# Performance work log

Hardware: AMD Instinct MI355X
Metric: run time of the kernel (lower is better)

The kernel has to match this reference:

```python
import jax, jax.numpy as jnp
from jax import lax
import numpy as np

# torch.sign(torch.sign(x) + 0.5): maps x<0 -> -1, x>=0 -> +1 (zeros go to +1)
def binarize(x):
    return jnp.where(x >= 0, 1.0, -1.0).astype(x.dtype)


def setup_inputs() -> dict:
    key = jax.random.key(0)
    kx, kw, kb = jax.random.split(key, 3)
    x = jax.random.normal(kx, (32, 256, 56, 56), dtype=jnp.float32)
    weight = jax.random.normal(kw, (256, 256, 3, 3), dtype=jnp.float32)
    bias = jax.random.normal(kb, (256,), dtype=jnp.float32)
    return {"x": x, "weight": weight, "bias": bias}


def reference(x, weight, bias):
    b_weight = binarize(weight)  # [O, I, kH, kW] in {-1, +1}
    b_bias = binarize(bias)      # [O] in {-1, +1}
    out = lax.conv_general_dilated(
        x, b_weight,
        window_strides=(1, 1),
        padding=((1, 1), (1, 1)),
        rhs_dilation=(1, 1),
        feature_group_count=1,
        dimension_numbers=("NCHW", "OIHW", "NCHW"),
    )
    return out + b_bias[None, :, None, None]
```

## Files before the change

kernel.cpp:

```cpp
#include <hip/hip_runtime.h>
#include <stdint.h>


#define N_IMG 32
#define C_IN  256
#define H_IN  56
#define W_IN  56
#define O_OUT 256
#define HW    (H_IN * W_IN)
#define K_RAW (C_IN * 9)

typedef int8_t i8x16 __attribute__((ext_vector_type(16)));
typedef int    i32x4 __attribute__((ext_vector_type(4)));
typedef float  f32x4 __attribute__((ext_vector_type(4)));
typedef __bf16 bf16x8 __attribute__((ext_vector_type(8)));

#define XQ_WSTR (58 * 64)
#define XQ_CSTR (58 * 58 * 64)
#define XQ_BYTES ((size_t)N_IMG * 4 * XQ_CSTR)
#define WQ_BYTES ((size_t)36 * 256 * 64)
#define AM_OFF   (XQ_BYTES + WQ_BYTES)
#define WS_NEED  (AM_OFF + 64)

#define BPITCH  80
#define BS_ROWB (58 * BPITCH)
#define APITCH  80

__global__ void amax_zero(unsigned* am) {
    if (threadIdx.x == 0 && blockIdx.x == 0) *am = 0u;
}

__global__ void amax_kernel(const float* __restrict__ x, unsigned* __restrict__ am) {
    const size_t NV = (size_t)N_IMG * C_IN * HW / 4;
    float m = 0.f;
    for (size_t i = (size_t)blockIdx.x * 256 + threadIdx.x; i < NV;
         i += (size_t)gridDim.x * 256) {
        f32x4 v = ((const f32x4*)x)[i];
        m = fmaxf(m, fmaxf(fmaxf(fabsf(v[0]), fabsf(v[1])),
                           fmaxf(fabsf(v[2]), fabsf(v[3]))));
    }
#pragma unroll
    for (int off = 32; off; off >>= 1)
        m = fmaxf(m, __shfl_down(m, off));
    __shared__ float red[4];
    if ((threadIdx.x & 63) == 0) red[threadIdx.x >> 6] = m;
    __syncthreads();
    if (threadIdx.x == 0) {
        m = fmaxf(fmaxf(red[0], red[1]), fmaxf(red[2], red[3]));
        atomicMax(am, __float_as_uint(m));
    }
}

__global__ void xtrans_q(const float* __restrict__ x, int8_t* __restrict__ xq,
                         const unsigned* __restrict__ amax_bits) {
    const int hh = blockIdx.x;
    const int cc = blockIdx.y;
    const int n  = blockIdx.z;
    const int t  = threadIdx.x;
    const int ww = t >> 2;
    const int cy = t & 3;
    if (ww >= 58) return;

    const float am    = __uint_as_float(*amax_bits);
    const float scale = 127.f / fmaxf(am, 1e-20f);

    i8x16 v;
    if (hh >= 1 && hh <= 56 && ww >= 1 && ww <= 56) {
        const float* src = x + ((size_t)n * C_IN + cc * 64 + cy * 16) * HW
                             + (hh - 1) * W_IN + (ww - 1);
#pragma unroll
        for (int j = 0; j < 16; ++j) {
            float f = src[(size_t)j * HW] * scale;
            f = fminf(fmaxf(f, -127.f), 127.f);
            v[j] = (int8_t)(int)rintf(f);
        }
    } else {
#pragma unroll
        for (int j = 0; j < 16; ++j) v[j] = 0;
    }
    *(i8x16*)(xq + ((size_t)(n * 4 + cc) * 3364 + hh * 58 + ww) * 64 + cy * 16) = v;
}

__global__ void wshuf_q(const float* __restrict__ w, int8_t* __restrict__ wq) {
    int idx = blockIdx.x * 256 + threadIdx.x;
    int cg  = idx & 3;
    int o   = (idx >> 2) & 255;
    int st  = idx >> 10;
    int tap = st % 9;
    int cc  = st / 9;
    i8x16 v;
#pragma unroll
    for (int j = 0; j < 16; ++j) {
        int ch = cc * 64 + cg * 16 + j;
        float f = w[(size_t)o * K_RAW + ch * 9 + tap];
        v[j] = (f >= 0.0f) ? (int8_t)1 : (int8_t)-1;
    }
    *(i8x16*)(wq + (size_t)idx * 16) = v;
}

__launch_bounds__(256, 2)
__global__ void bconv_i8(const int8_t* __restrict__ xq,
                         const int8_t* __restrict__ wq,
                         const float* __restrict__ bias,
                         const unsigned* __restrict__ amax_bits,
                         float* __restrict__ out) {
    __shared__ __attribute__((aligned(16))) int8_t Bs[6 * BS_ROWB];
    __shared__ __attribute__((aligned(16))) int8_t As[2][128 * APITCH];

    const int tid  = threadIdx.x;
    const int lane = tid & 63;
    const int wv   = tid >> 6;
    const int row  = lane & 15;
    const int quad = lane >> 4;

    const int nrp  = blockIdx.x;
    const int n    = nrp / 14;
    const int rp   = nrp - n * 14;
    const int oblk = blockIdx.y;
    const int h0   = rp * 4;

    int pr[4], pc[4];
    bool live[4];
#pragma unroll
    for (int nt = 0; nt < 4; ++nt) {
        int p = wv * 64 + nt * 16 + row;
        live[nt] = (p < 224);
        int r = p / 56;
        int c = p - r * 56;
        if (!live[nt]) { r = 0; c = 0; }
        pr[nt] = r;
        pc[nt] = c;
    }

    i32x4 acc[8][4];
#pragma unroll
    for (int mt = 0; mt < 8; ++mt)
#pragma unroll
        for (int nt = 0; nt < 4; ++nt)
            acc[mt][nt] = (i32x4){0, 0, 0, 0};

    i32x4 hreg[6];
    auto loadHalo = [&](int cc) {
        if (tid < 232) {
            const int8_t* bbase = xq + (size_t)(n * 4 + cc) * XQ_CSTR + (size_t)h0 * XQ_WSTR;
#pragma unroll
            for (int r6 = 0; r6 < 6; ++r6)
                hreg[r6] = *(const i32x4*)(bbase + r6 * XQ_WSTR + tid * 16);
        }
    };

    auto stageA = [&](int s, int buf) {
        const int8_t* asrc = wq + (size_t)s * 16384 + oblk * 8192;
#pragma unroll
        for (int it = 0; it < 2; ++it) {
            int idx = tid + it * 256;
            int o   = idx >> 2;
            int cg  = idx & 3;
            *(i32x4*)(&As[buf][o * APITCH + cg * 16]) =
                *(const i32x4*)(asrc + o * 64 + cg * 16);
        }
    };

    stageA(0, 0);
    loadHalo(0);

    for (int cc = 0; cc < 4; ++cc) {
        __syncthreads();
        if (tid < 232) {
            const int col = tid >> 2;
            const int cg  = tid & 3;
#pragma unroll
            for (int r6 = 0; r6 < 6; ++r6)
                *(i32x4*)(&Bs[r6 * BS_ROWB + col * BPITCH + cg * 16]) = hreg[r6];
        }
        if (cc < 3) loadHalo(cc + 1);

        for (int tap = 0; tap < 9; ++tap) {
            const int s = cc * 9 + tap;
            __syncthreads();
            if (s + 1 < 36) stageA(s + 1, (s + 1) & 1);

            const int dh = tap / 3;
            const int dw = tap - dh * 3;
            const int8_t* Ab = As[s & 1];

            i32x4 bfrag[4];
#pragma unroll
            for (int nt = 0; nt < 4; ++nt)
                bfrag[nt] = *(const i32x4*)(
                    &Bs[(pr[nt] + dh) * BS_ROWB + (pc[nt] + dw) * BPITCH + quad * 16]);
#pragma unroll
            for (int mt = 0; mt < 8; ++mt) {
                i32x4 af = *(const i32x4*)(&Ab[(mt * 16 + row) * APITCH + quad * 16]);
#pragma unroll
                for (int nt = 0; nt < 4; ++nt)
                    acc[mt][nt] = __builtin_amdgcn_mfma_i32_16x16x64_i8(
                        af, bfrag[nt], acc[mt][nt], 0, 0, 0);
            }
        }
    }

    const float am  = __uint_as_float(*amax_bits);
    const float inv = am * (1.0f / 127.0f);
#pragma unroll
    for (int nt = 0; nt < 4; ++nt) {
        if (!live[nt]) continue;
        float* obase = out + ((size_t)n * O_OUT + oblk * 128) * HW
                           + (h0 + pr[nt]) * W_IN + pc[nt];
#pragma unroll
        for (int mt = 0; mt < 8; ++mt) {
#pragma unroll
            for (int r = 0; r < 4; ++r) {
                int ol = mt * 16 + quad * 4 + r;
                float sb = (bias[oblk * 128 + ol] >= 0.0f) ? 1.0f : -1.0f;
                obase[(size_t)ol * HW] = (float)acc[mt][nt][r] * inv + sb;
            }
        }
    }
}

#define CHW (C_IN * HW)
#define FPITCH 40

__launch_bounds__(256, 2)
__global__ void bconv_fallback(const float* __restrict__ x,
                               const float* __restrict__ w,
                               const float* __restrict__ bias,
                               float* __restrict__ out) {
    __shared__ __attribute__((aligned(16))) __bf16 Asf[128 * FPITCH];
    __shared__ __attribute__((aligned(16))) __bf16 Bsf[128 * FPITCH];

    const int tid  = threadIdx.x;
    const int lane = tid & 63;
    const int wv   = tid >> 6;
    const int pblk = blockIdx.x;
    const int oblk = blockIdx.y;

    const int p_local = tid & 127;
    const int cgrp    = tid >> 7;
    const int pixel   = pblk * 128 + p_local;
    const int n_img   = pixel / HW;
    const int hw      = pixel - n_img * HW;
    const int h       = hw / W_IN;
    const int wx      = hw - h * W_IN;
    const float* xbase = x + (size_t)n_img * CHW;

    f32x4 acc[8][2];
#pragma unroll
    for (int mt = 0; mt < 8; ++mt)
#pragma unroll
        for (int nt = 0; nt < 2; ++nt)
            acc[mt][nt] = (f32x4){0.f, 0.f, 0.f, 0.f};

    const int pix_wave = wv * 32;
    const int row  = lane & 15;
    const int quad = lane >> 4;

    for (int tap = 0; tap < 9; ++tap) {
        const int dh = tap / 3 - 1;
        const int dw = tap % 3 - 1;
        const int hh = h + dh;
        const int ww = wx + dw;
        const bool valid = ((unsigned)hh < (unsigned)H_IN) && ((unsigned)ww < (unsigned)W_IN);
        const int offs = hh * W_IN + ww;

        for (int ck = 0; ck < 8; ++ck) {
            __syncthreads();
#pragma unroll
            for (int rep = 0; rep < 2; ++rep) {
                int v  = tid + rep * 256;
                int oa = v >> 2;
                int c8 = v & 3;
                const float* wsrc = w + (size_t)(oblk * 128 + oa) * K_RAW
                                      + (ck * 32 + c8 * 8) * 9 + tap;
                bf16x8 val;
#pragma unroll
                for (int j = 0; j < 8; ++j)
                    val[j] = (wsrc[j * 9] >= 0.0f) ? (__bf16)1.0f : (__bf16)(-1.0f);
                *(bf16x8*)(&Asf[oa * FPITCH + c8 * 8]) = val;
            }
            {
                const int cbase = (ck * 32 + cgrp * 16) * HW + offs;
#pragma unroll
                for (int g = 0; g < 2; ++g) {
                    bf16x8 vb;
#pragma unroll
                    for (int j = 0; j < 8; ++j) {
                        float f = valid ? xbase[cbase + (g * 8 + j) * HW] : 0.0f;
                        vb[j] = (__bf16)f;
                    }
                    *(bf16x8*)(&Bsf[p_local * FPITCH + cgrp * 16 + g * 8]) = vb;
                }
            }
            __syncthreads();
            bf16x8 bfrag[2];
#pragma unroll
            for (int nt = 0; nt < 2; ++nt)
                bfrag[nt] = *(const bf16x8*)(&Bsf[(pix_wave + nt * 16 + row) * FPITCH + quad * 8]);
#pragma unroll
            for (int mt = 0; mt < 8; ++mt) {
                bf16x8 afrag = *(const bf16x8*)(&Asf[(mt * 16 + row) * FPITCH + quad * 8]);
#pragma unroll
                for (int nt = 0; nt < 2; ++nt)
                    acc[mt][nt] = __builtin_amdgcn_mfma_f32_16x16x32_bf16(
                        afrag, bfrag[nt], acc[mt][nt], 0, 0, 0);
            }
        }
    }

#pragma unroll
    for (int nt = 0; nt < 2; ++nt) {
        int pix = pblk * 128 + pix_wave + nt * 16 + row;
        int ni  = pix / HW;
        int phw = pix - ni * HW;
        float* obase = out + (size_t)ni * (O_OUT * HW) + phw;
#pragma unroll
        for (int mt = 0; mt < 8; ++mt) {
            int o0 = oblk * 128 + mt * 16 + quad * 4;
#pragma unroll
            for (int r = 0; r < 4; ++r) {
                int o = o0 + r;
                float sb = (bias[o] >= 0.0f) ? 1.0f : -1.0f;
                obase[(size_t)o * HW] = acc[mt][nt][r] + sb;
            }
        }
    }
}

extern "C" void kernel_launch(void* const* d_in, const int* in_sizes, int n_in,
                              void* d_out, int out_size, void* d_ws, size_t ws_size,
                              hipStream_t stream) {
    const float* x    = (const float*)d_in[0];
    const float* w    = (const float*)d_in[1];
    const float* bias = (const float*)d_in[2];
    float* out        = (float*)d_out;

    if (ws_size >= WS_NEED) {
        int8_t*   xq = (int8_t*)d_ws;
        int8_t*   wq = (int8_t*)d_ws + XQ_BYTES;
        unsigned* am = (unsigned*)((char*)d_ws + AM_OFF);

        amax_zero<<<1, 64, 0, stream>>>(am);
        amax_kernel<<<1024, 256, 0, stream>>>(x, am);
        xtrans_q<<<dim3(58, 4, N_IMG), dim3(256), 0, stream>>>(x, xq, am);
        wshuf_q<<<144, 256, 0, stream>>>(w, (int8_t*)wq);
        bconv_i8<<<dim3(N_IMG * 14, 2), dim3(256), 0, stream>>>(xq, wq, bias, am, out);
    } else {
        bconv_fallback<<<dim3((N_IMG * HW) / 128, 2), dim3(256), 0, stream>>>(
            x, w, bias, out);
    }
}
```

Baseline: 321.3 us.

## Stage weight tiles via direct global-to-LDS DMA with swizzle and register prefetch

Weight tiles are now copied straight from global memory into LDS with global_load_lds instead of passing through registers. The padded LDS layout is replaced by a channel-group swizzle that is applied when the weights are shuffled, which avoids bank conflicts without padding. Fragments for the next tap are prefetched into registers while the current MFMAs run, and weight staging is issued two steps ahead. The halo prefetch across channel chunks is dropped in favour of a synchronous load, and the added register pressure and DMA ordering under the existing barriers carry some risk.

New measurement: 300.1 us. 6.6% less time.

```diff
diff --git a/kernel.cpp b/kernel.cpp
--- a/kernel.cpp
+++ b/kernel.cpp
@@ -24,7 +24,13 @@
 
 #define BPITCH  80
 #define BS_ROWB (58 * BPITCH)
-#define APITCH  80
+
+#define AS1 __attribute__((address_space(1)))
+#define AS3 __attribute__((address_space(3)))
+
+__device__ __forceinline__ void dma16(const void* g, void* l) {
+    __builtin_amdgcn_global_load_lds((const AS1 uint32_t*)g, (AS3 uint32_t*)l, 16, 0, 0);
+}
 
 __global__ void amax_zero(unsigned* am) {
     if (threadIdx.x == 0 && blockIdx.x == 0) *am = 0u;
@@ -82,16 +88,17 @@
 }
 
 __global__ void wshuf_q(const float* __restrict__ w, int8_t* __restrict__ wq) {
-    int idx = blockIdx.x * 256 + threadIdx.x;
-    int cg  = idx & 3;
-    int o   = (idx >> 2) & 255;
-    int st  = idx >> 10;
-    int tap = st % 9;
-    int cc  = st / 9;
+    int idx  = blockIdx.x * 256 + threadIdx.x;
+    int cpos = idx & 3;
+    int o    = (idx >> 2) & 255;
+    int st   = idx >> 10;
+    int tap  = st % 9;
+    int cc   = st / 9;
+    int truec = (cpos - ((o & 15) >> 1)) & 3;
     i8x16 v;
 #pragma unroll
     for (int j = 0; j < 16; ++j) {
-        int ch = cc * 64 + cg * 16 + j;
+        int ch = cc * 64 + truec * 16 + j;
         float f = w[(size_t)o * K_RAW + ch * 9 + tap];
         v[j] = (f >= 0.0f) ? (int8_t)1 : (int8_t)-1;
     }
@@ -104,8 +111,8 @@
                          const float* __restrict__ bias,
                          const unsigned* __restrict__ amax_bits,
                          float* __restrict__ out) {
+    __shared__ __attribute__((aligned(16))) int8_t As[2 * 8192];
     __shared__ __attribute__((aligned(16))) int8_t Bs[6 * BS_ROWB];
-    __shared__ __attribute__((aligned(16))) int8_t As[2][128 * APITCH];
 
     const int tid  = threadIdx.x;
     const int lane = tid & 63;
@@ -139,63 +146,78 @@
         for (int nt = 0; nt < 4; ++nt)
             acc[mt][nt] = (i32x4){0, 0, 0, 0};
 
-    i32x4 hreg[6];
-    auto loadHalo = [&](int cc) {
-        if (tid < 232) {
-            const int8_t* bbase = xq + (size_t)(n * 4 + cc) * XQ_CSTR + (size_t)h0 * XQ_WSTR;
-#pragma unroll
-            for (int r6 = 0; r6 < 6; ++r6)
-                hreg[r6] = *(const i32x4*)(bbase + r6 * XQ_WSTR + tid * 16);
-        }
+    const int rowA = row * 64 + (((quad + (row >> 1)) & 3) << 4);
+    int addrB[4];
+#pragma unroll
+    for (int nt = 0; nt < 4; ++nt)
+        addrB[nt] = pr[nt] * BS_ROWB + pc[nt] * BPITCH + quad * 16;
+
+    auto issueA = [&](int s) {
+        const int8_t* g = wq + (size_t)s * 16384 + oblk * 8192 + wv * 2048 + lane * 16;
+        int8_t* l = &As[(s & 1) * 8192 + wv * 2048];
+        dma16(g, l);
+        dma16(g + 1024, l + 1024);
     };
 
-    auto stageA = [&](int s, int buf) {
-        const int8_t* asrc = wq + (size_t)s * 16384 + oblk * 8192;
-#pragma unroll
-        for (int it = 0; it < 2; ++it) {
-            int idx = tid + it * 256;
-            int o   = idx >> 2;
-            int cg  = idx & 3;
-            *(i32x4*)(&As[buf][o * APITCH + cg * 16]) =
-                *(const i32x4*)(asrc + o * 64 + cg * 16);
-        }
-    };
-
-    stageA(0, 0);
-    loadHalo(0);
+    issueA(0);
+
+    i32x4 af[8], bc[4], bn[4];
 
     for (int cc = 0; cc < 4; ++cc) {
+        const int s0 = cc * 9;
         __syncthreads();
         if (tid < 232) {
-            const int col = tid >> 2;
-            const int cg  = tid & 3;
+            const int8_t* bbase = xq + (size_t)(n * 4 + cc) * XQ_CSTR
+                                     + (size_t)h0 * XQ_WSTR + tid * 16;
+            int8_t* ldst = &Bs[(tid >> 2) * BPITCH + (tid & 3) * 16];
+            i32x4 hv[6];
 #pragma unroll
             for (int r6 = 0; r6 < 6; ++r6)
-                *(i32x4*)(&Bs[r6 * BS_ROWB + col * BPITCH + cg * 16]) = hreg[r6];
-        }
-        if (cc < 3) loadHalo(cc + 1);
-
+                hv[r6] = *(const i32x4*)(bbase + r6 * XQ_WSTR);
+#pragma unroll
+            for (int r6 = 0; r6 < 6; ++r6)
+                *(i32x4*)(ldst + r6 * BS_ROWB) = hv[r6];
+        }
+        __syncthreads();
+        issueA(s0 + 1);
+
+        const int8_t* Acur = &As[(s0 & 1) * 8192];
+#pragma unroll
+        for (int mt = 0; mt < 8; ++mt)
+            af[mt] = *(const i32x4*)(Acur + mt * 1024 + rowA);
+#pragma unroll
+        for (int nt = 0; nt < 4; ++nt)
+            bc[nt] = *(const i32x4*)(&Bs[addrB[nt]]);
+
+#pragma unroll
         for (int tap = 0; tap < 9; ++tap) {
-            const int s = cc * 9 + tap;
-            __syncthreads();
-            if (s + 1 < 36) stageA(s + 1, (s + 1) & 1);
-
-            const int dh = tap / 3;
-            const int dw = tap - dh * 3;
-            const int8_t* Ab = As[s & 1];
-
-            i32x4 bfrag[4];
-#pragma unroll
-            for (int nt = 0; nt < 4; ++nt)
-                bfrag[nt] = *(const i32x4*)(
-                    &Bs[(pr[nt] + dh) * BS_ROWB + (pc[nt] + dw) * BPITCH + quad * 16]);
-#pragma unroll
-            for (int mt = 0; mt < 8; ++mt) {
-                i32x4 af = *(const i32x4*)(&Ab[(mt * 16 + row) * APITCH + quad * 16]);
+            const int s = s0 + tap;
+            if (tap < 8) {
+                __syncthreads();
+                if (s + 2 < 36) issueA(s + 2);
+                const int off2 = ((tap + 1) / 3) * BS_ROWB + ((tap + 1) % 3) * BPITCH;
 #pragma unroll
                 for (int nt = 0; nt < 4; ++nt)
-                    acc[mt][nt] = __builtin_amdgcn_mfma_i32_16x16x64_i8(
-                        af, bfrag[nt], acc[mt][nt], 0, 0, 0);
+                    bn[nt] = *(const i32x4*)(&Bs[addrB[nt] + off2]);
+                const int8_t* Anext = &As[((s + 1) & 1) * 8192];
+#pragma unroll
+                for (int mt = 0; mt < 8; ++mt) {
+                    i32x4 a = af[mt];
+#pragma unroll
+                    for (int nt = 0; nt < 4; ++nt)
+                        acc[mt][nt] = __builtin_amdgcn_mfma_i32_16x16x64_i8(
+                            a, bc[nt], acc[mt][nt], 0, 0, 0);
+                    af[mt] = *(const i32x4*)(Anext + mt * 1024 + rowA);
+                }
+#pragma unroll
+                for (int nt = 0; nt < 4; ++nt) bc[nt] = bn[nt];
+            } else {
+#pragma unroll
+                for (int mt = 0; mt < 8; ++mt)
+#pragma unroll
+                    for (int nt = 0; nt < 4; ++nt)
+                        acc[mt][nt] = __builtin_amdgcn_mfma_i32_16x16x64_i8(
+                            af[mt], bc[nt], acc[mt][nt], 0, 0, 0);
             }
         }
     }
@@ -343,7 +365,7 @@
         amax_zero<<<1, 64, 0, stream>>>(am);
         amax_kernel<<<1024, 256, 0, stream>>>(x, am);
         xtrans_q<<<dim3(58, 4, N_IMG), dim3(256), 0, stream>>>(x, xq, am);
-        wshuf_q<<<144, 256, 0, stream>>>(w, (int8_t*)wq);
+        wshuf_q<<<144, 256, 0, stream>>>(w, wq);
         bconv_i8<<<dim3(N_IMG * 14, 2), dim3(256), 0, stream>>>(xq, wq, bias, am, out);
     } else {
         bconv_fallback<<<dim3((N_IMG * HW) / 128, 2), dim3(256), 0, stream>>>(
```
